# Kernel tuning notes

Measured on AMD Instinct MI355X. Metric: run time of the kernel, lower is better.

## Reference

```python
import jax, jax.numpy as jnp
import numpy as np

B, T_ENC, T_DEC, E = 16, 512, 128, 512
H = 1024


def setup_inputs() -> dict:
    key = jax.random.key(0)
    ks = jax.random.split(key, 16)
    def rn(k, shape, s=0.02):
        return jax.random.normal(k, shape, jnp.float32) * s
    z = lambda *s: jnp.zeros(s, jnp.float32)
    return {
        "inputs": jax.random.normal(ks[0], (B, T_ENC, E), jnp.float32),
        "padded_mels": jax.random.normal(ks[1], (B, 80, T_DEC), jnp.float32),
        "W_enc": rn(ks[2], (128, E)),
        "W_q": rn(ks[3], (128, H)),
        "W_loc_conv": rn(ks[4], (32, 1, 31)),
        "b_loc_conv": z(32),
        "W_loc_dense": rn(ks[5], (128, 32)),
        "b_loc_dense": z(128),
        "w_e": rn(ks[6], (1, 128)),
        "b_e": z(1),
        "W_p1": rn(ks[7], (256, 80)),
        "W_p2": rn(ks[8], (256, 256)),
        "W_ih1": rn(ks[9], (4 * H, 256 + E)),
        "W_hh1": rn(ks[10], (4 * H, H)),
        "b_ih1": z(4 * H),
        "b_hh1": z(4 * H),
        "W_ih2": rn(ks[11], (4 * H, H)),
        "W_hh2": rn(ks[12], (4 * H, H)),
        "b_ih2": z(4 * H),
        "b_hh2": z(4 * H),
        "W_proj": rn(ks[13], (80, H + E)),
        "b_proj": z(80),
        "W_stop": rn(ks[14], (1, H + E)),
        "b_stop": z(1),
    }


def _lstm_cell(x, h, c, W_ih, W_hh, b_ih, b_hh):
    g = W_ih @ x + b_ih + W_hh @ h + b_hh
    i, f, gg, o = jnp.split(g, 4)  # torch gate order: i, f, g, o
    c = jax.nn.sigmoid(f) * c + jax.nn.sigmoid(i) * jnp.tanh(gg)
    h = jax.nn.sigmoid(o) * jnp.tanh(c)
    return h, c


def _forward(inputs, padded_mels, W_enc, W_q, W_loc_conv, b_loc_conv,
             W_loc_dense, b_loc_dense, w_e, b_e, W_p1, W_p2,
             W_ih1, W_hh1, b_ih1, b_hh1, W_ih2, W_hh2, b_ih2, b_hh2,
             W_proj, b_proj, W_stop, b_stop):
    proc_enc = inputs @ W_enc.T  # (B, T_enc, 128)
    # prepend zero frame, use frames 0..T_dec-1 as teacher-forced inputs
    prev = jnp.concatenate([jnp.zeros((B, 80, 1), inputs.dtype), padded_mels], axis=-1)[:, :, :T_DEC]
    prev = jnp.transpose(prev, (2, 0, 1))  # (T_dec, B, 80)
    # F.dropout(p=0.5) in source defaults to training=True -> always applied; deterministic masks here
    mk = jax.random.key(42)
    m1 = jax.random.bernoulli(jax.random.fold_in(mk, 0), 0.5, (T_DEC, B, 256)).astype(inputs.dtype) * 2.0
    m2 = jax.random.bernoulli(jax.random.fold_in(mk, 1), 0.5, (T_DEC, B, 256)).astype(inputs.dtype) * 2.0

    def lstm2(x_seq):
        # faithful to source: (B,1,768) fed to batch_first=False nn.LSTM ->
        # sequence runs over the batch dim with batch=1 and zero init state each step
        zv = jnp.zeros((H,), x_seq.dtype)
        def cell(carry, x):
            h1, c1, h2, c2 = carry
            h1, c1 = _lstm_cell(x, h1, c1, W_ih1, W_hh1, b_ih1, b_hh1)
            h2, c2 = _lstm_cell(h1, h2, c2, W_ih2, W_hh2, b_ih2, b_hh2)
            return (h1, c1, h2, c2), h2
        _, hs = jax.lax.scan(cell, (zv, zv, zv, zv), x_seq)
        return hs  # (B, 1024)

    def step(carry, xs):
        cum, ctx = carry  # (B, T_enc), (B, E)
        x, d1, d2 = xs
        p = jax.nn.relu(x @ W_p1.T) * d1
        p = jax.nn.relu(p @ W_p2.T) * d2
        h = lstm2(jnp.concatenate([p, ctx], axis=-1))  # (B, 1024)
        q = h @ W_q.T  # (B, 128)
        loc = jax.lax.conv_general_dilated(
            cum[:, None, :], W_loc_conv, (1,), [(15, 15)],
            dimension_numbers=("NCH", "OIH", "NCH")) + b_loc_conv[None, :, None]  # (B, 32, T_enc)
        loc = jnp.transpose(loc, (0, 2, 1)) @ W_loc_dense.T + b_loc_dense  # (B, T_enc, 128)
        e = jnp.tanh(q[:, None, :] + loc + proc_enc) @ w_e[0] + b_e[0]  # (B, T_enc)
        aw = jax.nn.softmax(e, axis=1)
        new_ctx = jnp.einsum("bt,bte->be", aw, inputs)  # (B, E)
        do = jnp.concatenate([h, new_ctx], axis=-1)  # (B, 1536)
        frame = do @ W_proj.T + b_proj  # (B, 80)
        stop = do @ W_stop[0] + b_stop[0]  # (B,)
        return (cum + aw, new_ctx), (frame, stop)

    carry0 = (jnp.zeros((B, T_ENC), inputs.dtype), jnp.zeros((B, E), inputs.dtype))
    _, (mels, stops) = jax.lax.scan(step, carry0, (prev, m1, m2))
    return jnp.transpose(mels, (1, 0, 2)), jnp.transpose(stops, (1, 0))


def reference(inputs, padded_mels, W_enc, W_q, W_loc_conv, b_loc_conv,
              W_loc_dense, b_loc_dense, w_e, b_e, W_p1, W_p2,
              W_ih1, W_hh1, b_ih1, b_hh1, W_ih2, W_hh2, b_ih2, b_hh2,
              W_proj, b_proj, W_stop, b_stop):
    return _forward(inputs, padded_mels, W_enc, W_q, W_loc_conv, b_loc_conv,
                    W_loc_dense, b_loc_dense, w_e, b_e, W_p1, W_p2,
                    W_ih1, W_hh1, b_ih1, b_hh1, W_ih2, W_hh2, b_ih2, b_hh2,
                    W_proj, b_proj, W_stop, b_stop)
```

## Files before the change

### kernel.cpp

```cpp
#include <hip/hip_runtime.h>
#include <hip/hip_bf16.h>
#include <stdint.h>

#define TD 128
#define NB 16
#define TE 512
#define EE 512
#define HH 1024
#define NM 80
#define PP 256
#define NWG 256
#define NTH 512

#define AGENT __HIP_MEMORY_SCOPE_AGENT

typedef float f32x4 __attribute__((ext_vector_type(4)));

__device__ inline void astoref(float* p, float v) {
  __hip_atomic_store(p, v, __ATOMIC_RELAXED, AGENT);
}
__device__ inline void astored(double* p, double v) {
  __hip_atomic_store(p, v, __ATOMIC_RELAXED, AGENT);
}
__device__ inline f32x4 ntload4(const float* p) {
  f32x4 r;
  asm volatile("global_load_dwordx4 %0, %1, off sc0\n\ts_waitcnt vmcnt(0)"
               : "=&v"(r) : "v"(p) : "memory");
  return r;
}
__device__ inline float ntload1f(const float* p) {
  float r;
  asm volatile("global_load_dword %0, %1, off sc0\n\ts_waitcnt vmcnt(0)"
               : "=&v"(r) : "v"(p) : "memory");
  return r;
}
__device__ inline double ntload1d(const double* p) {
  double r;
  asm volatile("global_load_dwordx2 %0, %1, off sc0\n\ts_waitcnt vmcnt(0)"
               : "=&v"(r) : "v"(p) : "memory");
  return r;
}
__device__ inline double dsig(double x) { return 1.0 / (1.0 + exp(-x)); }

__host__ __device__ inline void threefry2x32(uint32_t k0, uint32_t k1,
                                             uint32_t& x0, uint32_t& x1) {
  uint32_t ks0 = k0, ks1 = k1, ks2 = k0 ^ k1 ^ 0x1BD11BDAu;
  x0 += ks0; x1 += ks1;
#define RND(rot) { x0 += x1; x1 = (x1 << (rot)) | (x1 >> (32 - (rot))); x1 ^= x0; }
  RND(13) RND(15) RND(26) RND(6)
  x0 += ks1; x1 += ks2 + 1u;
  RND(17) RND(29) RND(16) RND(24)
  x0 += ks2; x1 += ks0 + 2u;
  RND(13) RND(15) RND(26) RND(6)
  x0 += ks0; x1 += ks1 + 3u;
  RND(17) RND(29) RND(16) RND(24)
  x0 += ks1; x1 += ks2 + 4u;
  RND(13) RND(15) RND(26) RND(6)
  x0 += ks2; x1 += ks0 + 5u;
#undef RND
}

__device__ inline double mask_val(uint32_t ka, uint32_t kb, uint32_t i) {
  uint32_t x0 = 0u, x1 = i;
  threefry2x32(ka, kb, x0, x1);
  uint32_t bits = x0 ^ x1;
  float u = __uint_as_float((bits >> 9) | 0x3f800000u) - 1.0f;
  return (u < 0.5f) ? 2.0 : 0.0;
}

__global__ void k_proc_enc(const float* __restrict__ inputs,
                           const float* __restrict__ W_enc,
                           float* __restrict__ procTf) {
  int blk = blockIdx.x;
  int b = blk >> 5;
  int t0 = (blk & 31) * 16;
  int d = threadIdx.x;
  __shared__ float in_l[16][EE];
  for (int idx = threadIdx.x; idx < 16 * EE; idx += blockDim.x) {
    int tt = idx >> 9, e = idx & 511;
    in_l[tt][e] = inputs[((size_t)(b * TE + t0 + tt)) * EE + e];
  }
  __syncthreads();
  double acc[16];
#pragma unroll
  for (int tt = 0; tt < 16; ++tt) acc[tt] = 0.0;
  const float* wr = W_enc + (size_t)d * EE;
  for (int e = 0; e < EE; ++e) {
    double w = (double)wr[e];
#pragma unroll
    for (int tt = 0; tt < 16; ++tt) acc[tt] += w * (double)in_l[tt][e];
  }
  for (int tt = 0; tt < 16; ++tt)
    procTf[((size_t)(b * 128 + d)) * TE + t0 + tt] = (float)acc[tt];
}

__global__ void k_p(const float* __restrict__ pm, const float* __restrict__ Wp1,
                    const float* __restrict__ Wp2,
                    uint32_t k1a, uint32_t k1b, uint32_t k2a, uint32_t k2b,
                    float* __restrict__ p_allf) {
  int sb = blockIdx.x;
  int s = sb >> 4, b = sb & 15;
  int tid = threadIdx.x;
  uint32_t mi = (uint32_t)(sb * PP + tid);
  double d1 = mask_val(k1a, k1b, mi);
  double d2 = mask_val(k2a, k2b, mi);
  __shared__ float x_l[NM];
  __shared__ double p1_l[PP];
  if (tid < NM) x_l[tid] = (s == 0) ? 0.f : pm[(b * NM + tid) * TD + (s - 1)];
  __syncthreads();
  double a = 0.0;
  const float* w1 = Wp1 + tid * NM;
  for (int m = 0; m < NM; ++m) a += (double)w1[m] * (double)x_l[m];
  a = fmax(a, 0.0) * d1;
  p1_l[tid] = a;
  __syncthreads();
  double c = 0.0;
  const float* w2 = Wp2 + tid * PP;
  for (int k = 0; k < PP; ++k) c += (double)w2[k] * p1_l[k];
  c = fmax(c, 0.0) * d2;
  p_allf[sb * PP + tid] = (float)c;
}

__global__ void k_init(double* __restrict__ cumg, float* __restrict__ ctxf,
                       float* __restrict__ h1f, float* __restrict__ h2f,
                       uint32_t* __restrict__ barmem) {
  int tid = threadIdx.x;
  for (int i = tid; i < NB * TE; i += 256) cumg[i] = 0.0;
  for (int i = tid; i < NB * EE; i += 256) ctxf[i] = 0.f;
  for (int i = tid; i < 2 * HH; i += 256) { h1f[i] = 0.f; h2f[i] = 0.f; }
  for (int i = tid; i < 8192; i += 256) barmem[i] = 0u;
}

struct SMEM {
  float wldT[4096];
  float wcl[992];
  double bld[128], we[128], blc[32];
  double b1l[16], b2l[16];
  double g1l[16][16];
  double gA[16], gBC[16];
  double c1l[4], c2l[4];
  double be0;
  union U {
    struct { float h1[1024], h2[1024]; } cell;
    struct { float h[1024]; } pq;
    struct { float ctxall[8192]; } g1p;
    struct { double cum[64], q[128], loc[32][33]; } att;
    struct { float aw[512]; double red[16][32]; } ctxp;
    struct { double red[16]; } soft;
    struct { float hb[1536]; double red[16]; } outp;
  } u;
};

__device__ inline void gridbar(uint32_t* barmem, uint32_t& lgen, int wg, int tid) {
  __syncthreads();
  lgen++;
  if (wg == 0) {
    if (tid == 0)
      (void)__hip_atomic_load(&barmem[0], __ATOMIC_ACQUIRE, AGENT);
    if (tid >= 256 && tid < 511) {
      const uint32_t* fl = &barmem[(tid - 255) * 16];
      while (__hip_atomic_load(fl, __ATOMIC_RELAXED, AGENT) < lgen)
        __builtin_amdgcn_s_sleep(1);
    }
    __syncthreads();
    if (tid < 256) {
      asm volatile("s_waitcnt vmcnt(0)" ::: "memory");
      __hip_atomic_store(&barmem[4096 + tid * 16], lgen, __ATOMIC_RELAXED, AGENT);
    }
  } else {
    if (tid == 0) {
      (void)__hip_atomic_load(&barmem[wg * 16], __ATOMIC_ACQUIRE, AGENT);
      __hip_atomic_store(&barmem[wg * 16], lgen, __ATOMIC_RELAXED, AGENT);
      while (__hip_atomic_load(&barmem[4096 + wg * 16], __ATOMIC_RELAXED, AGENT) < lgen)
        __builtin_amdgcn_s_sleep(1);
    }
  }
  __syncthreads();
}

__global__ __launch_bounds__(NTH)
__attribute__((amdgpu_waves_per_eu(2, 2)))
void k_persist(
    const float* __restrict__ inputs,
    const float* __restrict__ W_q,
    const float* __restrict__ W_lc, const float* __restrict__ b_lc,
    const float* __restrict__ W_ld, const float* __restrict__ b_ld,
    const float* __restrict__ w_e, const float* __restrict__ b_e,
    const float* __restrict__ W_ih1, const float* __restrict__ W_hh1,
    const float* __restrict__ b_ih1, const float* __restrict__ b_hh1,
    const float* __restrict__ W_ih2, const float* __restrict__ W_hh2,
    const float* __restrict__ b_ih2, const float* __restrict__ b_hh2,
    const float* __restrict__ W_proj, const float* __restrict__ b_proj,
    const float* __restrict__ W_stop, const float* __restrict__ b_stop,
    const float* __restrict__ p_allf, const float* __restrict__ procTf,
    float* h1f, float* h2f, float* h_allf, float* qf,
    float* ef, float* awf, double* cumg, float* ctxf,
    uint32_t* barmem, float* out) {
  __shared__ SMEM sm;
  const int wg = blockIdx.x, tid = threadIdx.x;
  const int q = tid >> 5, l = tid & 31;
  const int row = (q >> 2) * 1024 + wg * 4 + (q & 3);
  uint32_t lgen = 0;

  for (int i = tid; i < 4096; i += NTH) sm.wldT[(i & 31) * 128 + (i >> 5)] = W_ld[i];
  for (int i = tid; i < 992; i += NTH) sm.wcl[i] = W_lc[i];
  for (int i = tid; i < 128; i += NTH) { sm.bld[i] = (double)b_ld[i]; sm.we[i] = (double)w_e[i]; }
  if (tid < 32) sm.blc[tid] = (double)b_lc[tid];
  if (tid == 0) sm.be0 = (double)b_e[0];
  if (l == 0) {
    sm.b1l[q] = (double)b_ih1[row] + (double)b_hh1[row];
    sm.b2l[q] = (double)b_ih2[row] + (double)b_hh2[row];
  }

  float wA[32], wB[32], wC[32], wD[24];
#pragma unroll
  for (int k = 0; k < 32; ++k) {
    int c = l + 32 * k;
    wA[k] = W_hh1[(size_t)row * 1024 + c];
    wB[k] = W_ih2[(size_t)row * 1024 + c];
    wC[k] = W_hh2[(size_t)row * 1024 + c];
  }
#pragma unroll
  for (int k = 0; k < 24; ++k) wD[k] = W_ih1[(size_t)row * 768 + l + 32 * k];
#pragma unroll
  for (int k = 0; k < 32; ++k) {
    asm volatile("" : "+v"(wA[k]));
    asm volatile("" : "+v"(wB[k]));
    asm volatile("" : "+v"(wC[k]));
  }
#pragma unroll
  for (int k = 0; k < 24; ++k) asm volatile("" : "+v"(wD[k]));
  __syncthreads();

  {
    for (int j = 0; j < 4; ++j) {
      f32x4 v = ntload4(ctxf + (tid + j * NTH) * 4);
      *(f32x4*)&sm.u.g1p.ctxall[(tid + j * NTH) * 4] = v;
    }
    __syncthreads();
    for (int b = 0; b < 16; ++b) {
      double a = 0.0;
#pragma unroll
      for (int k = 0; k < 8; ++k)
        a += (double)wD[k] * (double)p_allf[((size_t)0 * 16 + b) * 256 + l + 32 * k];
#pragma unroll
      for (int k = 8; k < 24; ++k)
        a += (double)wD[k] * (double)sm.u.g1p.ctxall[b * 512 + l + 32 * k - 256];
#pragma unroll
      for (int m = 1; m <= 16; m <<= 1) a += __shfl_xor(a, m);
      if (l == 0) sm.g1l[b][q] = a + sm.b1l[q];
    }
    __syncthreads();
  }
  gridbar(barmem, lgen, wg, tid);

  for (int s = 0; s < TD; ++s) {
    for (int r = 0; r <= 16; ++r) {
      if (r == 0 && tid < 4) { sm.c1l[tid] = 0.0; sm.c2l[tid] = 0.0; }
      if (tid < 256) {
        f32x4 v = ntload4(h1f + (((r & 1) ^ 1)) * 1024 + tid * 4);
        *(f32x4*)&sm.u.cell.h1[tid * 4] = v;
      } else if (r > 0) {
        f32x4 v = ntload4(h2f + (r & 1) * 1024 + (tid - 256) * 4);
        *(f32x4*)&sm.u.cell.h2[(tid - 256) * 4] = v;
      }
      __syncthreads();

      double a0 = 0.0, a1 = 0.0, a2 = 0.0;
#pragma unroll
      for (int k = 0; k < 32; ++k) {
        double h1v = (double)sm.u.cell.h1[l + 32 * k];
        a0 += (double)wA[k] * h1v;
        a1 += (double)wB[k] * h1v;
        a2 += (double)wC[k] * (double)sm.u.cell.h2[l + 32 * k];
      }
#pragma unroll
      for (int m = 1; m <= 16; m <<= 1) {
        a0 += __shfl_xor(a0, m);
        a1 += __shfl_xor(a1, m);
        a2 += __shfl_xor(a2, m);
      }
      if (l == 0) { sm.gA[q] = a0; sm.gBC[q] = a1 + a2; }
      __syncthreads();

      if (r < 16 && tid < 4) {
        int jj = tid;
        double gi = sm.g1l[r][jj]      + sm.gA[jj];
        double gf = sm.g1l[r][4 + jj]  + sm.gA[4 + jj];
        double gg = sm.g1l[r][8 + jj]  + sm.gA[8 + jj];
        double go = sm.g1l[r][12 + jj] + sm.gA[12 + jj];
        double cn = dsig(gf) * sm.c1l[jj] + dsig(gi) * tanh(gg);
        double hn = dsig(go) * tanh(cn);
        sm.c1l[jj] = cn;
        astoref(h1f + (r & 1) * 1024 + wg * 4 + jj, (float)hn);
      }
      if (r > 0 && tid >= 8 && tid < 12) {
        int jj = tid - 8, b = r - 1;
        double gi = sm.gBC[jj]      + sm.b2l[jj];
        double gf = sm.gBC[4 + jj]  + sm.b2l[4 + jj];
        double gg = sm.gBC[8 + jj]  + sm.b2l[8 + jj];
        double go = sm.gBC[12 + jj] + sm.b2l[12 + jj];
        double cn = dsig(gf) * sm.c2l[jj] + dsig(gi) * tanh(gg);
        double hn = dsig(go) * tanh(cn);
        sm.c2l[jj] = cn;
        astoref(h2f + ((b & 1)) * 1024 + wg * 4 + jj, (float)hn);
        astoref(h_allf + (size_t)b * 1024 + wg * 4 + jj, (float)hn);
      }
      gridbar(barmem, lgen, wg, tid);
    }

    {
      int b = wg >> 4;
      if (tid < 256) {
        f32x4 v = ntload4(h_allf + (size_t)b * 1024 + tid * 4);
        *(f32x4*)&sm.u.pq.h[tid * 4] = v;
      }
      __syncthreads();
      int o = tid >> 6, lane = tid & 63;
      int d = (wg & 15) * 8 + o;
      double a = 0.0;
#pragma unroll
      for (int k = 0; k < 16; ++k) {
        int c = lane + 64 * k;
        a += (double)W_q[(size_t)d * 1024 + c] * (double)sm.u.pq.h[c];
      }
#pragma unroll
      for (int m = 1; m <= 32; m <<= 1) a += __shfl_xor(a, m);
      if (lane == 0) astoref(qf + b * 128 + d, (float)a);
    }
    gridbar(barmem, lgen, wg, tid);

    {
      int b = wg >> 4, t0 = (wg & 15) * 32;
      if (tid < 62) {
        int g = t0 - 15 + tid;
        sm.u.att.cum[tid] = (g >= 0 && g < TE) ? ntload1d(cumg + b * TE + g) : 0.0;
      } else if (tid < 190) {
        sm.u.att.q[tid - 62] = (double)ntload1f(qf + b * 128 + (tid - 62));
      }
      __syncthreads();
#pragma unroll
      for (int it = 0; it < 2; ++it) {
        int task = tid + it * NTH;
        int t = task >> 5, ch = task & 31;
        double v = sm.blc[ch];
#pragma unroll
        for (int k = 0; k < 31; ++k) v += (double)sm.wcl[ch * 31 + k] * sm.u.att.cum[t + k];
        sm.u.att.loc[t][ch] = v;
      }
      __syncthreads();
      int t = tid >> 4, part = tid & 15;
      double en = 0.0;
      for (int k = 0; k < 8; ++k) {
        int d = part + 16 * k;
        double sv = sm.u.att.q[d] + sm.bld[d] +
                    (double)procTf[((size_t)(b * 128 + d)) * TE + t0 + t];
#pragma unroll
        for (int c = 0; c < 32; ++c)
          sv += sm.u.att.loc[t][c] * (double)sm.wldT[c * 128 + d];
        en += tanh(sv) * sm.we[d];
      }
#pragma unroll
      for (int m = 1; m <= 8; m <<= 1) en += __shfl_xor(en, m);
      if (part == 0) astoref(ef + b * TE + t0 + t, (float)(en + sm.be0));
    }
    gridbar(barmem, lgen, wg, tid);

    if (wg < 16) {
      int b = wg;
      double e = (double)ntload1f(ef + b * TE + tid);
      double mx = e;
#pragma unroll
      for (int m = 1; m <= 32; m <<= 1) mx = fmax(mx, __shfl_xor(mx, m));
      if ((tid & 63) == 0) sm.u.soft.red[tid >> 6] = mx;
      __syncthreads();
      if (tid == 0) {
        double mm = sm.u.soft.red[0];
        for (int i = 1; i < 8; ++i) mm = fmax(mm, sm.u.soft.red[i]);
        sm.u.soft.red[0] = mm;
      }
      __syncthreads();
      double p = exp(e - sm.u.soft.red[0]);
      __syncthreads();
      double ssum = p;
#pragma unroll
      for (int m = 1; m <= 32; m <<= 1) ssum += __shfl_xor(ssum, m);
      if ((tid & 63) == 0) sm.u.soft.red[tid >> 6] = ssum;
      __syncthreads();
      if (tid == 0) {
        double t_ = 0.0;
        for (int i = 0; i < 8; ++i) t_ += sm.u.soft.red[i];
        sm.u.soft.red[0] = 1.0 / t_;
      }
      __syncthreads();
      double a = p * sm.u.soft.red[0];
      astoref(awf + b * TE + tid, (float)a);
      astored(cumg + b * TE + tid, ntload1d(cumg + b * TE + tid) + a);
    }
    gridbar(barmem, lgen, wg, tid);

    {
      int b = wg >> 4, e0 = (wg & 15) * 32;
      sm.u.ctxp.aw[tid] = ntload1f(awf + b * TE + tid);
      __syncthreads();
      int e = e0 + (tid & 31), tp = tid >> 5;
      double a = 0.0;
      for (int t = tp * 32; t < tp * 32 + 32; ++t)
        a += (double)sm.u.ctxp.aw[t] * (double)inputs[((size_t)(b * TE + t)) * EE + e];
      sm.u.ctxp.red[tp][tid & 31] = a;
      __syncthreads();
      if (tid < 32) {
        double v = 0.0;
        for (int j = 0; j < 16; ++j) v += sm.u.ctxp.red[j][tid];
        astoref(ctxf + b * EE + e0 + tid, (float)v);
      }
    }
    gridbar(barmem, lgen, wg, tid);

    {
      int b = wg & 15, obase = wg >> 4;
      if (tid < 256) {
        f32x4 v = ntload4(h_allf + (size_t)b * 1024 + tid * 4);
        *(f32x4*)&sm.u.outp.hb[tid * 4] = v;
      } else if (tid < 384) {
        f32x4 v = ntload4(ctxf + b * EE + (tid - 256) * 4);
        *(f32x4*)&sm.u.outp.hb[1024 + (tid - 256) * 4] = v;
      }
      __syncthreads();
      for (int j = 0; j < 6; ++j) {
        int o = obase + 16 * j;
        if (o <= NM) {
          const float* wr = (o < NM) ? (W_proj + (size_t)o * 1536) : W_stop;
          double a = 0.0;
#pragma unroll
          for (int kk = 0; kk < 3; ++kk) {
            int k = tid + kk * NTH;
            a += (double)wr[k] * (double)sm.u.outp.hb[k];
          }
#pragma unroll
          for (int m = 1; m <= 32; m <<= 1) a += __shfl_xor(a, m);
          if ((tid & 63) == 0) sm.u.outp.red[tid >> 6] = a;
          __syncthreads();
          if (tid == 0) {
            double v = 0.0;
            for (int i = 0; i < 8; ++i) v += sm.u.outp.red[i];
            v += (o < NM) ? (double)b_proj[o] : (double)b_stop[0];
            if (o < NM) astoref(out + ((size_t)b * TD + s) * NM + o, (float)v);
            else        astoref(out + (size_t)NB * TD * NM + b * TD + s, (float)v);
          }
          __syncthreads();
        }
      }
      __syncthreads();
      if (s < TD - 1) {
        const int ss = s + 1;
        for (int j = 0; j < 4; ++j) {
          f32x4 v = ntload4(ctxf + (tid + j * NTH) * 4);
          *(f32x4*)&sm.u.g1p.ctxall[(tid + j * NTH) * 4] = v;
        }
        __syncthreads();
        for (int b2 = 0; b2 < 16; ++b2) {
          double a = 0.0;
#pragma unroll
          for (int k = 0; k < 8; ++k)
            a += (double)wD[k] * (double)p_allf[((size_t)ss * 16 + b2) * 256 + l + 32 * k];
#pragma unroll
          for (int k = 8; k < 24; ++k)
            a += (double)wD[k] * (double)sm.u.g1p.ctxall[b2 * 512 + l + 32 * k - 256];
#pragma unroll
          for (int m = 1; m <= 16; m <<= 1) a += __shfl_xor(a, m);
          if (l == 0) sm.g1l[b2][q] = a + sm.b1l[q];
        }
        __syncthreads();
        if (tid < 4) astoref(h1f + 1024 + wg * 4 + tid, 0.f);
        else if (tid < 8) astoref(h2f + 1024 + wg * 4 + (tid - 4), 0.f);
      }
    }
    gridbar(barmem, lgen, wg, tid);
  }
}

extern "C" void kernel_launch(void* const* d_in, const int* in_sizes, int n_in,
                              void* d_out, int out_size, void* d_ws, size_t ws_size,
                              hipStream_t stream) {
  const float* inputs = (const float*)d_in[0];
  const float* pmels  = (const float*)d_in[1];
  const float* W_enc  = (const float*)d_in[2];
  const float* W_q    = (const float*)d_in[3];
  const float* W_lc   = (const float*)d_in[4];
  const float* b_lc   = (const float*)d_in[5];
  const float* W_ld   = (const float*)d_in[6];
  const float* b_ld   = (const float*)d_in[7];
  const float* w_e    = (const float*)d_in[8];
  const float* b_e    = (const float*)d_in[9];
  const float* W_p1   = (const float*)d_in[10];
  const float* W_p2   = (const float*)d_in[11];
  const float* W_ih1  = (const float*)d_in[12];
  const float* W_hh1  = (const float*)d_in[13];
  const float* b_ih1  = (const float*)d_in[14];
  const float* b_hh1  = (const float*)d_in[15];
  const float* W_ih2  = (const float*)d_in[16];
  const float* W_hh2  = (const float*)d_in[17];
  const float* b_ih2  = (const float*)d_in[18];
  const float* b_hh2  = (const float*)d_in[19];
  const float* W_proj = (const float*)d_in[20];
  const float* b_proj = (const float*)d_in[21];
  const float* W_stop = (const float*)d_in[22];
  const float* b_stop = (const float*)d_in[23];
  float* out = (float*)d_out;

  float* ws     = (float*)d_ws;
  float* p_allf = ws;
  float* procTf = p_allf + 524288;
  float* h1f    = procTf + 1048576;
  float* h2f    = h1f + 2048;
  float* h_allf = h2f + 2048;
  float* qf     = h_allf + 16384;
  float* ef     = qf + 2048;
  float* awf    = ef + 8192;
  float* ctxf   = awf + 8192;
  double* cumg  = (double*)(ctxf + 8192);
  uint32_t* barmem = (uint32_t*)(cumg + 8192);

  uint32_t k1a = 0u, k1b = 0u, k2a = 0u, k2b = 1u;
  threefry2x32(0u, 42u, k1a, k1b);
  threefry2x32(0u, 42u, k2a, k2b);

  k_proc_enc<<<512, 128, 0, stream>>>(inputs, W_enc, procTf);
  k_p<<<TD * NB, 256, 0, stream>>>(pmels, W_p1, W_p2, k1a, k1b, k2a, k2b, p_allf);
  k_init<<<1, 256, 0, stream>>>(cumg, ctxf, h1f, h2f, barmem);

  k_persist<<<NWG, NTH, 0, stream>>>(
      inputs, W_q, W_lc, b_lc, W_ld, b_ld, w_e, b_e,
      W_ih1, W_hh1, b_ih1, b_hh1, W_ih2, W_hh2, b_ih2, b_hh2,
      W_proj, b_proj, W_stop, b_stop,
      p_allf, procTf, h1f, h2f, h_allf, qf, ef, awf, cumg, ctxf,
      barmem, out);

  (void)in_sizes; (void)n_in; (void)out_size; (void)ws_size;
}
```

Before: 33.80 ms.

## Make grid barrier XCC-aware with one acquire per XCD captain

```diff
diff --git a/kernel.cpp b/kernel.cpp
--- a/kernel.cpp
+++ b/kernel.cpp
@@ -128,7 +128,7 @@
   for (int i = tid; i < NB * TE; i += 256) cumg[i] = 0.0;
   for (int i = tid; i < NB * EE; i += 256) ctxf[i] = 0.f;
   for (int i = tid; i < 2 * HH; i += 256) { h1f[i] = 0.f; h2f[i] = 0.f; }
-  for (int i = tid; i < 8192; i += 256) barmem[i] = 0u;
+  for (int i = tid; i < 8704; i += 256) barmem[i] = 0u;
 }
 
 struct SMEM {
@@ -140,6 +140,7 @@
   double gA[16], gBC[16];
   double c1l[4], c2l[4];
   double be0;
+  int myg, iscap;
   union U {
     struct { float h1[1024], h2[1024]; } cell;
     struct { float h[1024]; } pq;
@@ -151,12 +152,11 @@
   } u;
 };
 
-__device__ inline void gridbar(uint32_t* barmem, uint32_t& lgen, int wg, int tid) {
+
+__device__ inline void gridbar0(uint32_t* barmem, uint32_t& lgen, int wg, int tid) {
   __syncthreads();
   lgen++;
   if (wg == 0) {
-    if (tid == 0)
-      (void)__hip_atomic_load(&barmem[0], __ATOMIC_ACQUIRE, AGENT);
     if (tid >= 256 && tid < 511) {
       const uint32_t* fl = &barmem[(tid - 255) * 16];
       while (__hip_atomic_load(fl, __ATOMIC_RELAXED, AGENT) < lgen)
@@ -169,10 +169,47 @@
     }
   } else {
     if (tid == 0) {
-      (void)__hip_atomic_load(&barmem[wg * 16], __ATOMIC_ACQUIRE, AGENT);
       __hip_atomic_store(&barmem[wg * 16], lgen, __ATOMIC_RELAXED, AGENT);
       while (__hip_atomic_load(&barmem[4096 + wg * 16], __ATOMIC_RELAXED, AGENT) < lgen)
         __builtin_amdgcn_s_sleep(1);
+    }
+  }
+  __syncthreads();
+}
+
+__device__ inline void gridbar(uint32_t* barmem, uint32_t& lgen, int wg, int tid,
+                               int myg, int iscap) {
+  __syncthreads();
+  lgen++;
+  if (wg == 0) {
+    if (tid >= 256 && tid < 511) {
+      const uint32_t* fl = &barmem[(tid - 255) * 16];
+      while (__hip_atomic_load(fl, __ATOMIC_RELAXED, AGENT) < lgen)
+        __builtin_amdgcn_s_sleep(1);
+    }
+    __syncthreads();
+    if (tid < 256) {
+      asm volatile("s_waitcnt vmcnt(0)" ::: "memory");
+      __hip_atomic_store(&barmem[4096 + tid * 16], lgen, __ATOMIC_RELAXED, AGENT);
+    }
+    if (tid == 0) {
+      (void)__hip_atomic_load(&barmem[8192 + myg * 16], __ATOMIC_ACQUIRE, AGENT);
+      asm volatile("s_waitcnt vmcnt(0)" ::: "memory");
+      __hip_atomic_store(&barmem[8192 + myg * 16], lgen, __ATOMIC_RELAXED, AGENT);
+    }
+  } else {
+    if (tid == 0) {
+      __hip_atomic_store(&barmem[wg * 16], lgen, __ATOMIC_RELAXED, AGENT);
+      while (__hip_atomic_load(&barmem[4096 + wg * 16], __ATOMIC_RELAXED, AGENT) < lgen)
+        __builtin_amdgcn_s_sleep(1);
+      if (iscap) {
+        (void)__hip_atomic_load(&barmem[8192 + myg * 16], __ATOMIC_ACQUIRE, AGENT);
+        asm volatile("s_waitcnt vmcnt(0)" ::: "memory");
+        __hip_atomic_store(&barmem[8192 + myg * 16], lgen, __ATOMIC_RELAXED, AGENT);
+      } else {
+        while (__hip_atomic_load(&barmem[8192 + myg * 16], __ATOMIC_RELAXED, AGENT) < lgen)
+          __builtin_amdgcn_s_sleep(1);
+      }
     }
   }
   __syncthreads();
@@ -230,6 +267,12 @@
   }
 #pragma unroll
   for (int k = 0; k < 24; ++k) asm volatile("" : "+v"(wD[k]));
+
+  if (tid == 0) {
+    uint32_t xcc = (uint32_t)__builtin_amdgcn_s_getreg(20 | (31 << 11)) & 7u;
+    __hip_atomic_store(&barmem[8320 + wg], xcc, __ATOMIC_RELAXED, AGENT);
+    asm volatile("s_waitcnt vmcnt(0)" ::: "memory");
+  }
   __syncthreads();
 
   {
@@ -252,7 +295,20 @@
     }
     __syncthreads();
   }
-  gridbar(barmem, lgen, wg, tid);
+  gridbar0(barmem, lgen, wg, tid);
+
+  if (tid == 0) {
+    uint32_t myx = __hip_atomic_load(&barmem[8320 + wg], __ATOMIC_RELAXED, AGENT);
+    int cap = 1;
+    for (int w = 0; w < wg; ++w) {
+      if (__hip_atomic_load(&barmem[8320 + w], __ATOMIC_RELAXED, AGENT) == myx) {
+        cap = 0; break;
+      }
+    }
+    sm.myg = (int)myx; sm.iscap = cap;
+  }
+  __syncthreads();
+  const int myg = sm.myg, iscap = sm.iscap;
 
   for (int s = 0; s < TD; ++s) {
     for (int r = 0; r <= 16; ++r) {
@@ -306,7 +362,7 @@
         astoref(h2f + ((b & 1)) * 1024 + wg * 4 + jj, (float)hn);
         astoref(h_allf + (size_t)b * 1024 + wg * 4 + jj, (float)hn);
       }
-      gridbar(barmem, lgen, wg, tid);
+      gridbar(barmem, lgen, wg, tid, myg, iscap);
     }
 
     {
@@ -328,7 +384,7 @@
       for (int m = 1; m <= 32; m <<= 1) a += __shfl_xor(a, m);
       if (lane == 0) astoref(qf + b * 128 + d, (float)a);
     }
-    gridbar(barmem, lgen, wg, tid);
+    gridbar(barmem, lgen, wg, tid, myg, iscap);
 
     {
       int b = wg >> 4, t0 = (wg & 15) * 32;
@@ -364,7 +420,7 @@
       for (int m = 1; m <= 8; m <<= 1) en += __shfl_xor(en, m);
       if (part == 0) astoref(ef + b * TE + t0 + t, (float)(en + sm.be0));
     }
-    gridbar(barmem, lgen, wg, tid);
+    gridbar(barmem, lgen, wg, tid, myg, iscap);
 
     if (wg < 16) {
       int b = wg;
@@ -397,7 +453,7 @@
       astoref(awf + b * TE + tid, (float)a);
       astored(cumg + b * TE + tid, ntload1d(cumg + b * TE + tid) + a);
     }
-    gridbar(barmem, lgen, wg, tid);
+    gridbar(barmem, lgen, wg, tid, myg, iscap);
 
     {
       int b = wg >> 4, e0 = (wg & 15) * 32;
@@ -415,7 +471,7 @@
         astoref(ctxf + b * EE + e0 + tid, (float)v);
       }
     }
-    gridbar(barmem, lgen, wg, tid);
+    gridbar(barmem, lgen, wg, tid, myg, iscap);
 
     {
       int b = wg & 15, obase = wg >> 4;
@@ -476,7 +532,7 @@
         else if (tid < 8) astoref(h2f + 1024 + wg * 4 + (tid - 4), 0.f);
       }
     }
-    gridbar(barmem, lgen, wg, tid);
+    gridbar(barmem, lgen, wg, tid, myg, iscap);
   }
 }
 
```

Result: faster. 32.17 ms (-4.8%).

## Replicate shared recurrent state buffers across workgroup groups to spread cache traffic

Applied to the files above, without the earlier changes.

```diff
diff --git a/kernel.cpp b/kernel.cpp
--- a/kernel.cpp
+++ b/kernel.cpp
@@ -11,6 +11,7 @@
 #define PP 256
 #define NWG 256
 #define NTH 512
+#define NREP 8
 
 #define AGENT __HIP_MEMORY_SCOPE_AGENT
 
@@ -126,8 +127,8 @@
                        uint32_t* __restrict__ barmem) {
   int tid = threadIdx.x;
   for (int i = tid; i < NB * TE; i += 256) cumg[i] = 0.0;
-  for (int i = tid; i < NB * EE; i += 256) ctxf[i] = 0.f;
-  for (int i = tid; i < 2 * HH; i += 256) { h1f[i] = 0.f; h2f[i] = 0.f; }
+  for (int i = tid; i < NREP * NB * EE; i += 256) ctxf[i] = 0.f;
+  for (int i = tid; i < NREP * 2 * HH; i += 256) { h1f[i] = 0.f; h2f[i] = 0.f; }
   for (int i = tid; i < 8192; i += 256) barmem[i] = 0u;
 }
 
@@ -155,8 +156,6 @@
   __syncthreads();
   lgen++;
   if (wg == 0) {
-    if (tid == 0)
-      (void)__hip_atomic_load(&barmem[0], __ATOMIC_ACQUIRE, AGENT);
     if (tid >= 256 && tid < 511) {
       const uint32_t* fl = &barmem[(tid - 255) * 16];
       while (__hip_atomic_load(fl, __ATOMIC_RELAXED, AGENT) < lgen)
@@ -169,7 +168,6 @@
     }
   } else {
     if (tid == 0) {
-      (void)__hip_atomic_load(&barmem[wg * 16], __ATOMIC_ACQUIRE, AGENT);
       __hip_atomic_store(&barmem[wg * 16], lgen, __ATOMIC_RELAXED, AGENT);
       while (__hip_atomic_load(&barmem[4096 + wg * 16], __ATOMIC_RELAXED, AGENT) < lgen)
         __builtin_amdgcn_s_sleep(1);
@@ -200,6 +198,7 @@
   const int wg = blockIdx.x, tid = threadIdx.x;
   const int q = tid >> 5, l = tid & 31;
   const int row = (q >> 2) * 1024 + wg * 4 + (q & 3);
+  const int rep = wg & (NREP - 1);
   uint32_t lgen = 0;
 
   for (int i = tid; i < 4096; i += NTH) sm.wldT[(i & 31) * 128 + (i >> 5)] = W_ld[i];
@@ -234,7 +233,7 @@
 
   {
     for (int j = 0; j < 4; ++j) {
-      f32x4 v = ntload4(ctxf + (tid + j * NTH) * 4);
+      f32x4 v = ntload4(ctxf + rep * 8192 + (tid + j * NTH) * 4);
       *(f32x4*)&sm.u.g1p.ctxall[(tid + j * NTH) * 4] = v;
     }
     __syncthreads();
@@ -258,10 +257,10 @@
     for (int r = 0; r <= 16; ++r) {
       if (r == 0 && tid < 4) { sm.c1l[tid] = 0.0; sm.c2l[tid] = 0.0; }
       if (tid < 256) {
-        f32x4 v = ntload4(h1f + (((r & 1) ^ 1)) * 1024 + tid * 4);
+        f32x4 v = ntload4(h1f + rep * 2048 + (((r & 1) ^ 1)) * 1024 + tid * 4);
         *(f32x4*)&sm.u.cell.h1[tid * 4] = v;
       } else if (r > 0) {
-        f32x4 v = ntload4(h2f + (r & 1) * 1024 + (tid - 256) * 4);
+        f32x4 v = ntload4(h2f + rep * 2048 + (r & 1) * 1024 + (tid - 256) * 4);
         *(f32x4*)&sm.u.cell.h2[(tid - 256) * 4] = v;
       }
       __syncthreads();
@@ -292,7 +291,10 @@
         double cn = dsig(gf) * sm.c1l[jj] + dsig(gi) * tanh(gg);
         double hn = dsig(go) * tanh(cn);
         sm.c1l[jj] = cn;
-        astoref(h1f + (r & 1) * 1024 + wg * 4 + jj, (float)hn);
+        float hf = (float)hn;
+#pragma unroll
+        for (int g = 0; g < NREP; ++g)
+          astoref(h1f + g * 2048 + (r & 1) * 1024 + wg * 4 + jj, hf);
       }
       if (r > 0 && tid >= 8 && tid < 12) {
         int jj = tid - 8, b = r - 1;
@@ -303,8 +305,12 @@
         double cn = dsig(gf) * sm.c2l[jj] + dsig(gi) * tanh(gg);
         double hn = dsig(go) * tanh(cn);
         sm.c2l[jj] = cn;
-        astoref(h2f + ((b & 1)) * 1024 + wg * 4 + jj, (float)hn);
-        astoref(h_allf + (size_t)b * 1024 + wg * 4 + jj, (float)hn);
+        float hf = (float)hn;
+#pragma unroll
+        for (int g = 0; g < NREP; ++g) {
+          astoref(h2f + g * 2048 + (b & 1) * 1024 + wg * 4 + jj, hf);
+          astoref(h_allf + g * 16384 + (size_t)b * 1024 + wg * 4 + jj, hf);
+        }
       }
       gridbar(barmem, lgen, wg, tid);
     }
@@ -312,7 +318,7 @@
     {
       int b = wg >> 4;
       if (tid < 256) {
-        f32x4 v = ntload4(h_allf + (size_t)b * 1024 + tid * 4);
+        f32x4 v = ntload4(h_allf + rep * 16384 + (size_t)b * 1024 + tid * 4);
         *(f32x4*)&sm.u.pq.h[tid * 4] = v;
       }
       __syncthreads();
@@ -326,7 +332,12 @@
       }
 #pragma unroll
       for (int m = 1; m <= 32; m <<= 1) a += __shfl_xor(a, m);
-      if (lane == 0) astoref(qf + b * 128 + d, (float)a);
+      if (lane == 0) {
+        float qv = (float)a;
+#pragma unroll
+        for (int g = 0; g < NREP; ++g)
+          astoref(qf + g * 2048 + b * 128 + d, qv);
+      }
     }
     gridbar(barmem, lgen, wg, tid);
 
@@ -336,7 +347,7 @@
         int g = t0 - 15 + tid;
         sm.u.att.cum[tid] = (g >= 0 && g < TE) ? ntload1d(cumg + b * TE + g) : 0.0;
       } else if (tid < 190) {
-        sm.u.att.q[tid - 62] = (double)ntload1f(qf + b * 128 + (tid - 62));
+        sm.u.att.q[tid - 62] = (double)ntload1f(qf + rep * 2048 + b * 128 + (tid - 62));
       }
       __syncthreads();
 #pragma unroll
@@ -394,14 +405,17 @@
       }
       __syncthreads();
       double a = p * sm.u.soft.red[0];
-      astoref(awf + b * TE + tid, (float)a);
+      float av = (float)a;
+#pragma unroll
+      for (int g = 0; g < NREP; ++g)
+        astoref(awf + g * 8192 + b * TE + tid, av);
       astored(cumg + b * TE + tid, ntload1d(cumg + b * TE + tid) + a);
     }
     gridbar(barmem, lgen, wg, tid);
 
     {
       int b = wg >> 4, e0 = (wg & 15) * 32;
-      sm.u.ctxp.aw[tid] = ntload1f(awf + b * TE + tid);
+      sm.u.ctxp.aw[tid] = ntload1f(awf + rep * 8192 + b * TE + tid);
       __syncthreads();
       int e = e0 + (tid & 31), tp = tid >> 5;
       double a = 0.0;
@@ -412,7 +426,10 @@
       if (tid < 32) {
         double v = 0.0;
         for (int j = 0; j < 16; ++j) v += sm.u.ctxp.red[j][tid];
-        astoref(ctxf + b * EE + e0 + tid, (float)v);
+        float cv = (float)v;
+#pragma unroll
+        for (int g = 0; g < NREP; ++g)
+          astoref(ctxf + g * 8192 + b * EE + e0 + tid, cv);
       }
     }
     gridbar(barmem, lgen, wg, tid);
@@ -420,10 +437,10 @@
     {
       int b = wg & 15, obase = wg >> 4;
       if (tid < 256) {
-        f32x4 v = ntload4(h_allf + (size_t)b * 1024 + tid * 4);
+        f32x4 v = ntload4(h_allf + rep * 16384 + (size_t)b * 1024 + tid * 4);
         *(f32x4*)&sm.u.outp.hb[tid * 4] = v;
       } else if (tid < 384) {
-        f32x4 v = ntload4(ctxf + b * EE + (tid - 256) * 4);
+        f32x4 v = ntload4(ctxf + rep * 8192 + b * EE + (tid - 256) * 4);
         *(f32x4*)&sm.u.outp.hb[1024 + (tid - 256) * 4] = v;
       }
       __syncthreads();
@@ -455,7 +472,7 @@
       if (s < TD - 1) {
         const int ss = s + 1;
         for (int j = 0; j < 4; ++j) {
-          f32x4 v = ntload4(ctxf + (tid + j * NTH) * 4);
+          f32x4 v = ntload4(ctxf + rep * 8192 + (tid + j * NTH) * 4);
           *(f32x4*)&sm.u.g1p.ctxall[(tid + j * NTH) * 4] = v;
         }
         __syncthreads();
@@ -472,8 +489,15 @@
           if (l == 0) sm.g1l[b2][q] = a + sm.b1l[q];
         }
         __syncthreads();
-        if (tid < 4) astoref(h1f + 1024 + wg * 4 + tid, 0.f);
-        else if (tid < 8) astoref(h2f + 1024 + wg * 4 + (tid - 4), 0.f);
+        if (tid < 4) {
+#pragma unroll
+          for (int g = 0; g < NREP; ++g)
+            astoref(h1f + g * 2048 + 1024 + wg * 4 + tid, 0.f);
+        } else if (tid < 8) {
+#pragma unroll
+          for (int g = 0; g < NREP; ++g)
+            astoref(h2f + g * 2048 + 1024 + wg * 4 + (tid - 4), 0.f);
+        }
       }
     }
     gridbar(barmem, lgen, wg, tid);
@@ -513,13 +537,13 @@
   float* p_allf = ws;
   float* procTf = p_allf + 524288;
   float* h1f    = procTf + 1048576;
-  float* h2f    = h1f + 2048;
-  float* h_allf = h2f + 2048;
-  float* qf     = h_allf + 16384;
-  float* ef     = qf + 2048;
+  float* h2f    = h1f + NREP * 2048;
+  float* h_allf = h2f + NREP * 2048;
+  float* qf     = h_allf + NREP * 16384;
+  float* ef     = qf + NREP * 2048;
   float* awf    = ef + 8192;
-  float* ctxf   = awf + 8192;
-  double* cumg  = (double*)(ctxf + 8192);
+  float* ctxf   = awf + NREP * 8192;
+  double* cumg  = (double*)(ctxf + NREP * 8192);
   uint32_t* barmem = (uint32_t*)(cumg + 8192);
 
   uint32_t k1a = 0u, k1b = 0u, k2a = 0u, k2b = 1u;
```

Result: slower. 36.33 ms (+7.5%).

## Exchange LSTM hidden states in fp16 and vectorize global loads in persistent kernel

Applied to the files above, without the earlier changes.

```diff
diff --git a/kernel.cpp b/kernel.cpp
--- a/kernel.cpp
+++ b/kernel.cpp
@@ -1,5 +1,6 @@
 #include <hip/hip_runtime.h>
 #include <hip/hip_bf16.h>
+#include <hip/hip_fp16.h>
 #include <stdint.h>
 
 #define TD 128
@@ -22,23 +23,43 @@
 __device__ inline void astored(double* p, double v) {
   __hip_atomic_store(p, v, __ATOMIC_RELAXED, AGENT);
 }
-__device__ inline f32x4 ntload4(const float* p) {
+__device__ inline void astoreh2(uint16_t* p, float a, float b) {
+  __half2 h = __floats2half2_rn(a, b);
+  union { __half2 h; uint32_t u; } c; c.h = h;
+  __hip_atomic_store((uint32_t*)p, c.u, __ATOMIC_RELAXED, AGENT);
+}
+__device__ inline f32x4 ntload4(const void* p) {
   f32x4 r;
   asm volatile("global_load_dwordx4 %0, %1, off sc0\n\ts_waitcnt vmcnt(0)"
                : "=&v"(r) : "v"(p) : "memory");
   return r;
 }
-__device__ inline float ntload1f(const float* p) {
-  float r;
-  asm volatile("global_load_dword %0, %1, off sc0\n\ts_waitcnt vmcnt(0)"
-               : "=&v"(r) : "v"(p) : "memory");
-  return r;
+__device__ inline void ntload4x4(const float* p0, const float* p1,
+                                 const float* p2, const float* p3,
+                                 f32x4& a, f32x4& b, f32x4& c, f32x4& d) {
+  asm volatile(
+      "global_load_dwordx4 %0, %4, off sc0\n\t"
+      "global_load_dwordx4 %1, %5, off sc0\n\t"
+      "global_load_dwordx4 %2, %6, off sc0\n\t"
+      "global_load_dwordx4 %3, %7, off sc0\n\t"
+      "s_waitcnt vmcnt(0)"
+      : "=&v"(a), "=&v"(b), "=&v"(c), "=&v"(d)
+      : "v"(p0), "v"(p1), "v"(p2), "v"(p3) : "memory");
 }
 __device__ inline double ntload1d(const double* p) {
   double r;
   asm volatile("global_load_dwordx2 %0, %1, off sc0\n\ts_waitcnt vmcnt(0)"
                : "=&v"(r) : "v"(p) : "memory");
   return r;
+}
+__device__ inline void unpack8(f32x4 raw, float* dst) {
+  union { f32x4 f; uint32_t u[4]; } c; c.f = raw;
+#pragma unroll
+  for (int j = 0; j < 4; ++j) {
+    union { uint32_t u; __half2 h; } w; w.u = c.u[j];
+    float2 f2 = __half22float2(w.h);
+    dst[2 * j] = f2.x; dst[2 * j + 1] = f2.y;
+  }
 }
 __device__ inline double dsig(double x) { return 1.0 / (1.0 + exp(-x)); }
 
@@ -122,12 +143,12 @@
 }
 
 __global__ void k_init(double* __restrict__ cumg, float* __restrict__ ctxf,
-                       float* __restrict__ h1f, float* __restrict__ h2f,
+                       uint32_t* __restrict__ h1h, uint32_t* __restrict__ h2h,
                        uint32_t* __restrict__ barmem) {
   int tid = threadIdx.x;
   for (int i = tid; i < NB * TE; i += 256) cumg[i] = 0.0;
   for (int i = tid; i < NB * EE; i += 256) ctxf[i] = 0.f;
-  for (int i = tid; i < 2 * HH; i += 256) { h1f[i] = 0.f; h2f[i] = 0.f; }
+  for (int i = tid; i < 1024; i += 256) { h1h[i] = 0u; h2h[i] = 0u; }
   for (int i = tid; i < 8192; i += 256) barmem[i] = 0u;
 }
 
@@ -146,7 +167,7 @@
     struct { float ctxall[8192]; } g1p;
     struct { double cum[64], q[128], loc[32][33]; } att;
     struct { float aw[512]; double red[16][32]; } ctxp;
-    struct { double red[16]; } soft;
+    struct { float est[512]; double red[16]; } soft;
     struct { float hb[1536]; double red[16]; } outp;
   } u;
 };
@@ -155,8 +176,6 @@
   __syncthreads();
   lgen++;
   if (wg == 0) {
-    if (tid == 0)
-      (void)__hip_atomic_load(&barmem[0], __ATOMIC_ACQUIRE, AGENT);
     if (tid >= 256 && tid < 511) {
       const uint32_t* fl = &barmem[(tid - 255) * 16];
       while (__hip_atomic_load(fl, __ATOMIC_RELAXED, AGENT) < lgen)
@@ -169,7 +188,6 @@
     }
   } else {
     if (tid == 0) {
-      (void)__hip_atomic_load(&barmem[wg * 16], __ATOMIC_ACQUIRE, AGENT);
       __hip_atomic_store(&barmem[wg * 16], lgen, __ATOMIC_RELAXED, AGENT);
       while (__hip_atomic_load(&barmem[4096 + wg * 16], __ATOMIC_RELAXED, AGENT) < lgen)
         __builtin_amdgcn_s_sleep(1);
@@ -193,7 +211,7 @@
     const float* __restrict__ W_proj, const float* __restrict__ b_proj,
     const float* __restrict__ W_stop, const float* __restrict__ b_stop,
     const float* __restrict__ p_allf, const float* __restrict__ procTf,
-    float* h1f, float* h2f, float* h_allf, float* qf,
+    uint16_t* h1h, uint16_t* h2h, uint16_t* h_allh, float* qf,
     float* ef, float* awf, double* cumg, float* ctxf,
     uint32_t* barmem, float* out) {
   __shared__ SMEM sm;
@@ -233,22 +251,25 @@
   __syncthreads();
 
   {
-    for (int j = 0; j < 4; ++j) {
-      f32x4 v = ntload4(ctxf + (tid + j * NTH) * 4);
-      *(f32x4*)&sm.u.g1p.ctxall[(tid + j * NTH) * 4] = v;
-    }
+    f32x4 a, b, c, d;
+    ntload4x4(ctxf + tid * 4, ctxf + (tid + NTH) * 4,
+              ctxf + (tid + 2 * NTH) * 4, ctxf + (tid + 3 * NTH) * 4, a, b, c, d);
+    *(f32x4*)&sm.u.g1p.ctxall[tid * 4] = a;
+    *(f32x4*)&sm.u.g1p.ctxall[(tid + NTH) * 4] = b;
+    *(f32x4*)&sm.u.g1p.ctxall[(tid + 2 * NTH) * 4] = c;
+    *(f32x4*)&sm.u.g1p.ctxall[(tid + 3 * NTH) * 4] = d;
     __syncthreads();
-    for (int b = 0; b < 16; ++b) {
-      double a = 0.0;
+    for (int b2 = 0; b2 < 16; ++b2) {
+      double a2 = 0.0;
 #pragma unroll
       for (int k = 0; k < 8; ++k)
-        a += (double)wD[k] * (double)p_allf[((size_t)0 * 16 + b) * 256 + l + 32 * k];
+        a2 += (double)wD[k] * (double)p_allf[((size_t)0 * 16 + b2) * 256 + l + 32 * k];
 #pragma unroll
       for (int k = 8; k < 24; ++k)
-        a += (double)wD[k] * (double)sm.u.g1p.ctxall[b * 512 + l + 32 * k - 256];
-#pragma unroll
-      for (int m = 1; m <= 16; m <<= 1) a += __shfl_xor(a, m);
-      if (l == 0) sm.g1l[b][q] = a + sm.b1l[q];
+        a2 += (double)wD[k] * (double)sm.u.g1p.ctxall[b2 * 512 + l + 32 * k - 256];
+#pragma unroll
+      for (int m = 1; m <= 16; m <<= 1) a2 += __shfl_xor(a2, m);
+      if (l == 0) sm.g1l[b2][q] = a2 + sm.b1l[q];
     }
     __syncthreads();
   }
@@ -257,12 +278,12 @@
   for (int s = 0; s < TD; ++s) {
     for (int r = 0; r <= 16; ++r) {
       if (r == 0 && tid < 4) { sm.c1l[tid] = 0.0; sm.c2l[tid] = 0.0; }
-      if (tid < 256) {
-        f32x4 v = ntload4(h1f + (((r & 1) ^ 1)) * 1024 + tid * 4);
-        *(f32x4*)&sm.u.cell.h1[tid * 4] = v;
-      } else if (r > 0) {
-        f32x4 v = ntload4(h2f + (r & 1) * 1024 + (tid - 256) * 4);
-        *(f32x4*)&sm.u.cell.h2[(tid - 256) * 4] = v;
+      if (tid < 128) {
+        f32x4 v = ntload4(h1h + (((r & 1) ^ 1)) * 1024 + tid * 8);
+        unpack8(v, &sm.u.cell.h1[tid * 8]);
+      } else if (tid < 256 && r > 0) {
+        f32x4 v = ntload4(h2h + (r & 1) * 1024 + (tid - 128) * 8);
+        unpack8(v, &sm.u.cell.h2[(tid - 128) * 8]);
       }
       __syncthreads();
 
@@ -283,37 +304,49 @@
       if (l == 0) { sm.gA[q] = a0; sm.gBC[q] = a1 + a2; }
       __syncthreads();
 
-      if (r < 16 && tid < 4) {
-        int jj = tid;
-        double gi = sm.g1l[r][jj]      + sm.gA[jj];
-        double gf = sm.g1l[r][4 + jj]  + sm.gA[4 + jj];
-        double gg = sm.g1l[r][8 + jj]  + sm.gA[8 + jj];
-        double go = sm.g1l[r][12 + jj] + sm.gA[12 + jj];
-        double cn = dsig(gf) * sm.c1l[jj] + dsig(gi) * tanh(gg);
-        double hn = dsig(go) * tanh(cn);
-        sm.c1l[jj] = cn;
-        astoref(h1f + (r & 1) * 1024 + wg * 4 + jj, (float)hn);
-      }
-      if (r > 0 && tid >= 8 && tid < 12) {
-        int jj = tid - 8, b = r - 1;
-        double gi = sm.gBC[jj]      + sm.b2l[jj];
-        double gf = sm.gBC[4 + jj]  + sm.b2l[4 + jj];
-        double gg = sm.gBC[8 + jj]  + sm.b2l[8 + jj];
-        double go = sm.gBC[12 + jj] + sm.b2l[12 + jj];
-        double cn = dsig(gf) * sm.c2l[jj] + dsig(gi) * tanh(gg);
-        double hn = dsig(go) * tanh(cn);
-        sm.c2l[jj] = cn;
-        astoref(h2f + ((b & 1)) * 1024 + wg * 4 + jj, (float)hn);
-        astoref(h_allf + (size_t)b * 1024 + wg * 4 + jj, (float)hn);
+      if (r < 16 && tid < 2) {
+        int jj0 = tid * 2;
+        float hf[2];
+#pragma unroll
+        for (int e = 0; e < 2; ++e) {
+          int jj = jj0 + e;
+          double gi = sm.g1l[r][jj]      + sm.gA[jj];
+          double gf = sm.g1l[r][4 + jj]  + sm.gA[4 + jj];
+          double gg = sm.g1l[r][8 + jj]  + sm.gA[8 + jj];
+          double go = sm.g1l[r][12 + jj] + sm.gA[12 + jj];
+          double cn = dsig(gf) * sm.c1l[jj] + dsig(gi) * tanh(gg);
+          double hn = dsig(go) * tanh(cn);
+          sm.c1l[jj] = cn;
+          hf[e] = (float)hn;
+        }
+        astoreh2(h1h + (r & 1) * 1024 + wg * 4 + jj0, hf[0], hf[1]);
+      }
+      if (r > 0 && tid >= 8 && tid < 10) {
+        int jj0 = (tid - 8) * 2, b = r - 1;
+        float hf[2];
+#pragma unroll
+        for (int e = 0; e < 2; ++e) {
+          int jj = jj0 + e;
+          double gi = sm.gBC[jj]      + sm.b2l[jj];
+          double gf = sm.gBC[4 + jj]  + sm.b2l[4 + jj];
+          double gg = sm.gBC[8 + jj]  + sm.b2l[8 + jj];
+          double go = sm.gBC[12 + jj] + sm.b2l[12 + jj];
+          double cn = dsig(gf) * sm.c2l[jj] + dsig(gi) * tanh(gg);
+          double hn = dsig(go) * tanh(cn);
+          sm.c2l[jj] = cn;
+          hf[e] = (float)hn;
+        }
+        astoreh2(h2h + (b & 1) * 1024 + wg * 4 + jj0, hf[0], hf[1]);
+        astoreh2(h_allh + (size_t)b * 1024 + wg * 4 + jj0, hf[0], hf[1]);
       }
       gridbar(barmem, lgen, wg, tid);
     }
 
     {
       int b = wg >> 4;
-      if (tid < 256) {
-        f32x4 v = ntload4(h_allf + (size_t)b * 1024 + tid * 4);
-        *(f32x4*)&sm.u.pq.h[tid * 4] = v;
+      if (tid < 128) {
+        f32x4 v = ntload4(h_allh + (size_t)b * 1024 + tid * 8);
+        unpack8(v, &sm.u.pq.h[tid * 8]);
       }
       __syncthreads();
       int o = tid >> 6, lane = tid & 63;
@@ -335,8 +368,10 @@
       if (tid < 62) {
         int g = t0 - 15 + tid;
         sm.u.att.cum[tid] = (g >= 0 && g < TE) ? ntload1d(cumg + b * TE + g) : 0.0;
-      } else if (tid < 190) {
-        sm.u.att.q[tid - 62] = (double)ntload1f(qf + b * 128 + (tid - 62));
+      } else if (tid >= 64 && tid < 96) {
+        f32x4 v = ntload4(qf + b * 128 + (tid - 64) * 4);
+#pragma unroll
+        for (int j = 0; j < 4; ++j) sm.u.att.q[(tid - 64) * 4 + j] = (double)v[j];
       }
       __syncthreads();
 #pragma unroll
@@ -368,7 +403,12 @@
 
     if (wg < 16) {
       int b = wg;
-      double e = (double)ntload1f(ef + b * TE + tid);
+      if (tid < 128) {
+        f32x4 v = ntload4(ef + b * TE + tid * 4);
+        *(f32x4*)&sm.u.soft.est[tid * 4] = v;
+      }
+      __syncthreads();
+      double e = (double)sm.u.soft.est[tid];
       double mx = e;
 #pragma unroll
       for (int m = 1; m <= 32; m <<= 1) mx = fmax(mx, __shfl_xor(mx, m));
@@ -401,7 +441,10 @@
 
     {
       int b = wg >> 4, e0 = (wg & 15) * 32;
-      sm.u.ctxp.aw[tid] = ntload1f(awf + b * TE + tid);
+      if (tid < 128) {
+        f32x4 v = ntload4(awf + b * TE + tid * 4);
+        *(f32x4*)&sm.u.ctxp.aw[tid * 4] = v;
+      }
       __syncthreads();
       int e = e0 + (tid & 31), tp = tid >> 5;
       double a = 0.0;
@@ -419,12 +462,12 @@
 
     {
       int b = wg & 15, obase = wg >> 4;
-      if (tid < 256) {
-        f32x4 v = ntload4(h_allf + (size_t)b * 1024 + tid * 4);
-        *(f32x4*)&sm.u.outp.hb[tid * 4] = v;
-      } else if (tid < 384) {
-        f32x4 v = ntload4(ctxf + b * EE + (tid - 256) * 4);
-        *(f32x4*)&sm.u.outp.hb[1024 + (tid - 256) * 4] = v;
+      if (tid < 128) {
+        f32x4 v = ntload4(h_allh + (size_t)b * 1024 + tid * 8);
+        unpack8(v, &sm.u.outp.hb[tid * 8]);
+      } else if (tid < 256) {
+        f32x4 v = ntload4(ctxf + b * EE + (tid - 128) * 4);
+        *(f32x4*)&sm.u.outp.hb[1024 + (tid - 128) * 4] = v;
       }
       __syncthreads();
       for (int j = 0; j < 6; ++j) {
@@ -454,10 +497,14 @@
       __syncthreads();
       if (s < TD - 1) {
         const int ss = s + 1;
-        for (int j = 0; j < 4; ++j) {
-          f32x4 v = ntload4(ctxf + (tid + j * NTH) * 4);
-          *(f32x4*)&sm.u.g1p.ctxall[(tid + j * NTH) * 4] = v;
-        }
+        f32x4 va, vb, vc, vd;
+        ntload4x4(ctxf + tid * 4, ctxf + (tid + NTH) * 4,
+                  ctxf + (tid + 2 * NTH) * 4, ctxf + (tid + 3 * NTH) * 4,
+                  va, vb, vc, vd);
+        *(f32x4*)&sm.u.g1p.ctxall[tid * 4] = va;
+        *(f32x4*)&sm.u.g1p.ctxall[(tid + NTH) * 4] = vb;
+        *(f32x4*)&sm.u.g1p.ctxall[(tid + 2 * NTH) * 4] = vc;
+        *(f32x4*)&sm.u.g1p.ctxall[(tid + 3 * NTH) * 4] = vd;
         __syncthreads();
         for (int b2 = 0; b2 < 16; ++b2) {
           double a = 0.0;
@@ -472,8 +519,8 @@
           if (l == 0) sm.g1l[b2][q] = a + sm.b1l[q];
         }
         __syncthreads();
-        if (tid < 4) astoref(h1f + 1024 + wg * 4 + tid, 0.f);
-        else if (tid < 8) astoref(h2f + 1024 + wg * 4 + (tid - 4), 0.f);
+        if (tid < 2) astoreh2(h1h + 1024 + wg * 4 + tid * 2, 0.f, 0.f);
+        else if (tid < 4) astoreh2(h2h + 1024 + wg * 4 + (tid - 2) * 2, 0.f, 0.f);
       }
     }
     gridbar(barmem, lgen, wg, tid);
@@ -509,17 +556,17 @@
   const float* b_stop = (const float*)d_in[23];
   float* out = (float*)d_out;
 
-  float* ws     = (float*)d_ws;
-  float* p_allf = ws;
-  float* procTf = p_allf + 524288;
-  float* h1f    = procTf + 1048576;
-  float* h2f    = h1f + 2048;
-  float* h_allf = h2f + 2048;
-  float* qf     = h_allf + 16384;
-  float* ef     = qf + 2048;
-  float* awf    = ef + 8192;
-  float* ctxf   = awf + 8192;
-  double* cumg  = (double*)(ctxf + 8192);
+  float* ws      = (float*)d_ws;
+  float* p_allf  = ws;
+  float* procTf  = p_allf + 524288;
+  uint16_t* h1h  = (uint16_t*)(procTf + 1048576);
+  uint16_t* h2h  = h1h + 2048;
+  uint16_t* h_allh = h2h + 2048;
+  float* qf      = (float*)(h_allh + 16384);
+  float* ef      = qf + 2048;
+  float* awf     = ef + 8192;
+  float* ctxf    = awf + 8192;
+  double* cumg   = (double*)(ctxf + 8192);
   uint32_t* barmem = (uint32_t*)(cumg + 8192);
 
   uint32_t k1a = 0u, k1b = 0u, k2a = 0u, k2b = 1u;
@@ -528,13 +575,13 @@
 
   k_proc_enc<<<512, 128, 0, stream>>>(inputs, W_enc, procTf);
   k_p<<<TD * NB, 256, 0, stream>>>(pmels, W_p1, W_p2, k1a, k1b, k2a, k2b, p_allf);
-  k_init<<<1, 256, 0, stream>>>(cumg, ctxf, h1f, h2f, barmem);
+  k_init<<<1, 256, 0, stream>>>(cumg, ctxf, (uint32_t*)h1h, (uint32_t*)h2h, barmem);
 
   k_persist<<<NWG, NTH, 0, stream>>>(
       inputs, W_q, W_lc, b_lc, W_ld, b_ld, w_e, b_e,
       W_ih1, W_hh1, b_ih1, b_hh1, W_ih2, W_hh2, b_ih2, b_hh2,
       W_proj, b_proj, W_stop, b_stop,
-      p_allf, procTf, h1f, h2f, h_allf, qf, ef, awf, cumg, ctxf,
+      p_allf, procTf, h1h, h2h, h_allh, qf, ef, awf, cumg, ctxf,
       barmem, out);
 
   (void)in_sizes; (void)n_in; (void)out_size; (void)ws_size;
```

New measurement: 42.06 ms. +24.4%, slower.
